# Kernel tuning notes

Measured on AMD Instinct MI355X. Metric: run time of the kernel, lower is better.

## Reference

```python
import jax, jax.numpy as jnp
import numpy as np

EPS = 1e-12
BIG_NEG = 1e10
SPARSE_RATIO = 0.5
ATTN_W = 0.8
KEEPED = 39          # int(196 * 0.4 * 0.5)
HIDDEN = 102         # int(512 * 0.2)
DIM = 512


def l2norm(x, axis=-1):
    n = jnp.sqrt(jnp.sum(x * x, axis=axis, keepdims=True))
    return x / jnp.maximum(n, EPS)


def layernorm(x, g, b):
    mu = jnp.mean(x, axis=-1, keepdims=True)
    var = jnp.mean(jnp.square(x - mu), axis=-1, keepdims=True)
    return (x - mu) / jnp.sqrt(var + 1e-5) * g + b


def token_aggregation(x, ln_g, ln_b, W1, b1, W2, b2, scale):
    # x: [B, L, C] -> [B, K, C]
    h = layernorm(x, ln_g, ln_b)
    h = jax.nn.gelu(h @ W1 + b1, approximate=False)
    w = h @ W2 + b2                       # [B, L, K]
    w = jnp.swapaxes(w, 1, 2) * scale     # [B, K, L]
    w = jax.nn.softmax(w, axis=2)
    return jnp.einsum('bkl,blc->bkc', w, x)


def setup_inputs() -> dict:
    key = jax.random.key(0)
    ks = jax.random.split(key, 8)
    B_v, L_v, B_t, L_t = 256, 197, 256, 64
    inp = {
        'img_embs': jax.random.normal(ks[0], (B_v, L_v, DIM), jnp.float32),
        'cap_embs': jax.random.normal(ks[1], (B_t, L_t, DIM), jnp.float32),
        'cap_lens': jax.random.randint(ks[2], (B_t,), 8, L_t + 1),
        'ln_g': jnp.ones((DIM,), jnp.float32),
        'ln_b': jnp.zeros((DIM,), jnp.float32),
        'W1': jax.random.normal(ks[3], (DIM, HIDDEN), jnp.float32) * 0.02,
        'b1': jnp.zeros((HIDDEN,), jnp.float32),
        'W2': jax.random.normal(ks[4], (HIDDEN, KEEPED), jnp.float32) * 0.02,
        'b2': jnp.zeros((KEEPED,), jnp.float32),
        'scale': jnp.ones((1, 1, 1), jnp.float32),
    }
    return inp


def reference(img_embs, cap_embs, cap_lens, ln_g, ln_b, W1, b1, W2, b2, scale):
    B_v = img_embs.shape[0]
    L_t = cap_embs.shape[1]
    num_keep = int(KEEPED * SPARSE_RATIO)  # 19

    # CLS split (197 is not a perfect square -> has_cls_token)
    img_cls = img_embs[:, 0:1, :]
    spatial = img_embs[:, 1:, :]

    aggr = token_aggregation(spatial, ln_g, ln_b, W1, b1, W2, b2, scale)  # [B_v, 39, C]
    aggr_norm = l2norm(aggr)
    cap_norm = l2norm(cap_embs)

    glo = jax.lax.stop_gradient(l2norm(jnp.mean(aggr, axis=1, keepdims=True)))
    att_self = jax.lax.stop_gradient(jnp.sum(glo * aggr_norm, axis=-1))  # [B_v, 39]

    word_mask = (jnp.arange(L_t)[None, :] < cap_lens[:, None]).astype(img_embs.dtype)

    def one_caption(cap_i, cap_i_norm, m):
        nw = jnp.sum(m)
        cap_glo = jax.lax.stop_gradient(
            l2norm(jnp.sum(cap_i * m[:, None], axis=0) / nw))        # [C]
        att_y = jax.lax.stop_gradient(
            jnp.sum(cap_glo * aggr_norm, axis=-1))                    # [B_v, 39]
        score = ATTN_W * att_y + (1.0 - ATTN_W) * att_self
        _, idx = jax.lax.top_k(score, num_keep)                       # [B_v, 19]
        select = jnp.take_along_axis(aggr, idx[:, :, None], axis=1)   # [B_v, 19, C]
        score_mask = jnp.zeros_like(score).at[
            jnp.arange(B_v)[:, None], idx].set(1.0)                   # [B_v, 39]
        w_drop = jax.nn.softmax(score - score_mask * BIG_NEG, axis=-1)
        extra = jnp.einsum('bl,blc->bc', w_drop, aggr)[:, None, :]    # [B_v, 1, C]
        sel = l2norm(jnp.concatenate([img_cls, select, extra], axis=1))  # [B_v, 21, C]
        sim = jnp.einsum('wc,bkc->bwk', cap_i_norm, sel)              # [B_v, L_t, 21]
        sim_max = jnp.max(sim, axis=-1)                               # [B_v, L_t]
        sim_text = jnp.sum(sim_max * m, axis=-1) / nw                 # [B_v]
        return sim_text, score_mask

    sims, score_mask_all = jax.vmap(one_caption)(cap_embs, cap_norm, word_mask)
    return sims.T  # [B_v, B_t]
```

## Files before the change

kernel.cpp:

```cpp
#include <hip/hip_runtime.h>
#include <hip/hip_bf16.h>
#include <cfloat>
#include <cmath>

typedef float f32x4 __attribute__((ext_vector_type(4)));
typedef float f32x2 __attribute__((ext_vector_type(2)));
typedef short bf16x8 __attribute__((ext_vector_type(8)));

#define HID 102
#define KEEPN 39
#define DIMD 512

static __device__ __forceinline__ unsigned int f2bf(float v) {
  unsigned int b = __float_as_uint(v);
  return (b + 0x7FFFu + ((b >> 16) & 1u)) >> 16;
}
static __device__ __forceinline__ float wsum(float v) {
#pragma unroll
  for (int m = 1; m < 64; m <<= 1) v += __shfl_xor(v, m, 64);
  return v;
}
static __device__ __forceinline__ float wmaxr(float v) {
#pragma unroll
  for (int m = 1; m < 64; m <<= 1) v = fmaxf(v, __shfl_xor(v, m, 64));
  return v;
}
static __device__ __forceinline__ float bsum(float v, float* red4, int lane, int wid) {
  v = wsum(v);
  if (lane == 0) red4[wid] = v;
  __syncthreads();
  float r = red4[0] + red4[1] + red4[2] + red4[3];
  __syncthreads();
  return r;
}

__global__ __launch_bounds__(256) void k0_prep(
    const float* __restrict__ W1, const float* __restrict__ b1,
    const float* __restrict__ W2, const float* __restrict__ lng,
    const float* __restrict__ lnb,
    float* __restrict__ w1gT, float* __restrict__ b1eff, float* __restrict__ w2T) {
  int tid = blockIdx.x * 256 + threadIdx.x;
  for (int idx = tid; idx < HID * DIMD; idx += (int)gridDim.x * 256) {
    int c = idx >> 9, k = idx & 511;
    w1gT[idx] = lng[k] * W1[k * HID + c];
  }
  for (int idx = tid; idx < KEEPN * 104; idx += (int)gridDim.x * 256) {
    int l = idx / 104, k = idx - l * 104;
    w2T[idx] = (k < HID) ? W2[k * KEEPN + l] : 0.0f;
  }
  if (blockIdx.x == 0 && threadIdx.x < 104) {
    int c = threadIdx.x;
    float s = 0.f;
    if (c < HID) {
      s = b1[c];
      for (int k = 0; k < DIMD; ++k) s += lnb[k] * W1[k * HID + c];
    }
    b1eff[c] = s;
  }
}

__global__ __launch_bounds__(256, 2) void k1a(
    const float* __restrict__ img, const float* __restrict__ w1gT,
    const float* __restrict__ b1eff, const float* __restrict__ w2T,
    const float* __restrict__ b2, const float* __restrict__ scale,
    float* __restrict__ wmat) {
  int b = blockIdx.x;
  int tid = threadIdx.x;
  int lane = tid & 63, wid = tid >> 6;
  __shared__ float mu_s[196], rs_s[196];
  __shared__ __attribute__((aligned(16))) float w2t_s[KEEPN * 104];
  __shared__ float b1e_s[104];
  __shared__ __attribute__((aligned(16))) float uni[6864];
  float* x_s = uni;
  float* w1g_s = uni + 2176;
  float* h1_s = uni;
  const float* xb = img + (size_t)b * 197 * DIMD + DIMD;
  float scv = scale[0];
  for (int u = tid; u < KEEPN * 104 / 4; u += 256)
    ((f32x4*)w2t_s)[u] = ((const f32x4*)w2T)[u];
  if (tid < 104) b1e_s[tid] = b1eff[tid];
#pragma unroll 1
  for (int it = 0; it < 49; ++it) {
    int t = it * 4 + wid;
    const float* xr = xb + (size_t)t * DIMD + lane * 8;
    f32x4 v0 = *(const f32x4*)xr;
    f32x4 v1 = *(const f32x4*)(xr + 4);
    float s = v0[0]+v0[1]+v0[2]+v0[3]+v1[0]+v1[1]+v1[2]+v1[3];
    float q = v0[0]*v0[0]+v0[1]*v0[1]+v0[2]*v0[2]+v0[3]*v0[3]
            + v1[0]*v1[0]+v1[1]*v1[1]+v1[2]*v1[2]+v1[3]*v1[3];
    s = wsum(s); q = wsum(q);
    if (lane == 0) {
      float mu = s * (1.f/512.f);
      float var = q * (1.f/512.f) - mu*mu;
      mu_s[t] = mu;
      rs_s[t] = 1.f / sqrtf(var + 1e-5f);
    }
  }
  __syncthreads();
  int kh = tid >> 7, r = tid & 127, tg = r & 15, cg = r >> 4;
#pragma unroll 1
  for (int t0 = 0; t0 < 196; t0 += 64) {
    float acc[4][13] = {};
#pragma unroll 1
    for (int kc = 0; kc < DIMD; kc += 32) {
      __syncthreads();
#pragma unroll
      for (int j = 0; j < 2; ++j) {
        int u = tid + 256 * j;
        int tt = u >> 3, f = u & 7;
        int t = t0 + tt;
        if (t < 196) {
          f32x4 v = *(const f32x4*)(xb + (size_t)t * DIMD + kc + 4*f);
          float mu = mu_s[t], rs = rs_s[t];
          x_s[(4*f+0)*68 + tt] = (v[0]-mu)*rs;
          x_s[(4*f+1)*68 + tt] = (v[1]-mu)*rs;
          x_s[(4*f+2)*68 + tt] = (v[2]-mu)*rs;
          x_s[(4*f+3)*68 + tt] = (v[3]-mu)*rs;
        }
      }
#pragma unroll
      for (int j = 0; j < 4; ++j) {
        int u = tid + 256 * j;
        if (u < 816) {
          int c = u >> 3, f = u & 7;
          *(f32x4*)&w1g_s[c*36 + 4*f] = *(const f32x4*)(w1gT + c*DIMD + kc + 4*f);
        }
      }
      __syncthreads();
#pragma unroll
      for (int k4 = 0; k4 < 4; ++k4) {
        int kk = kh*16 + k4*4;
        f32x4 a0 = *(const f32x4*)&x_s[(kk+0)*68 + 4*tg];
        f32x4 a1 = *(const f32x4*)&x_s[(kk+1)*68 + 4*tg];
        f32x4 a2 = *(const f32x4*)&x_s[(kk+2)*68 + 4*tg];
        f32x4 a3 = *(const f32x4*)&x_s[(kk+3)*68 + 4*tg];
#pragma unroll
        for (int ci = 0; ci < 13; ++ci) {
          f32x4 w = *(const f32x4*)&w1g_s[(cg*13+ci)*36 + kk];
#pragma unroll
          for (int t = 0; t < 4; ++t)
            acc[t][ci] += a0[t]*w[0] + a1[t]*w[1] + a2[t]*w[2] + a3[t]*w[3];
        }
      }
    }
    __syncthreads();
    if (kh == 1) {
#pragma unroll
      for (int ci = 0; ci < 13; ++ci) {
        int c = cg*13 + ci;
        if (c < HID)
#pragma unroll
          for (int t = 0; t < 4; ++t) h1_s[c*66 + 4*tg + t] = acc[t][ci];
      }
    }
    __syncthreads();
    if (kh == 0) {
#pragma unroll
      for (int ci = 0; ci < 13; ++ci) {
        int c = cg*13 + ci;
        if (c < HID)
#pragma unroll
          for (int t = 0; t < 4; ++t) {
            float v = h1_s[c*66 + 4*tg + t] + acc[t][ci] + b1e_s[c];
            v = 0.5f * v * (1.f + erff(v * 0.70710678118654752f));
            h1_s[c*66 + 4*tg + t] = v;
          }
      }
    }
    if (tid < 128) h1_s[(HID + (tid >> 6))*66 + (tid & 63)] = 0.f;
    __syncthreads();
    {
      int t4 = tid & 31, lg = tid >> 5;
      int nl = (lg == 7) ? 4 : 5;
      float a2c[2][5] = {};
#pragma unroll 2
      for (int k = 0; k < 104; k += 4) {
        f32x4 wvv[5];
#pragma unroll
        for (int li = 0; li < 5; ++li) {
          if (li < nl) wvv[li] = *(const f32x4*)&w2t_s[(lg*5+li)*104 + k];
          else wvv[li] = (f32x4){0.f,0.f,0.f,0.f};
        }
#pragma unroll
        for (int j = 0; j < 4; ++j) {
          f32x2 h = *(const f32x2*)&h1_s[(k+j)*66 + 2*t4];
#pragma unroll
          for (int li = 0; li < 5; ++li) {
            a2c[0][li] += h[0]*wvv[li][j];
            a2c[1][li] += h[1]*wvv[li][j];
          }
        }
      }
#pragma unroll
      for (int li = 0; li < 5; ++li) {
        if (li < nl) {
          int l = lg*5 + li;
          float bb = b2[l];
#pragma unroll
          for (int tp = 0; tp < 2; ++tp) {
            int t = t0 + 2*t4 + tp;
            if (t < 196) wmat[((size_t)b*KEEPN + l)*196 + t] = (a2c[tp][li] + bb) * scv;
          }
        }
      }
    }
  }
}

__global__ __launch_bounds__(256) void k1agg(
    const float* __restrict__ img, const float* __restrict__ wmat,
    float* __restrict__ agn, unsigned short* __restrict__ bm,
    float* __restrict__ na_g, float* __restrict__ gloraw) {
  int b = blockIdx.x, tid = threadIdx.x;
  int lane = tid & 63, wid = tid >> 6;
  __shared__ __attribute__((aligned(16))) float wm_s[KEEPN * 200];
  __shared__ float red_s[13 * 4];
  __shared__ float na_s[13];
  for (int u = tid; u < KEEPN * 49; u += 256) {
    int l = u / 49, t4 = u - l * 49;
    *(f32x4*)&wm_s[l*200 + 4*t4] = *(const f32x4*)(wmat + ((size_t)b*KEEPN + l)*196 + 4*t4);
  }
  __syncthreads();
  for (int l = wid; l < KEEPN; l += 4) {
    float v0 = wm_s[l*200 + lane];
    float v1 = wm_s[l*200 + 64 + lane];
    float v2 = wm_s[l*200 + 128 + lane];
    float v3 = (lane < 4) ? wm_s[l*200 + 192 + lane] : -FLT_MAX;
    float mx = wmaxr(fmaxf(fmaxf(v0, v1), fmaxf(v2, v3)));
    float e0 = expf(v0 - mx), e1 = expf(v1 - mx), e2 = expf(v2 - mx);
    float e3 = (lane < 4) ? expf(v3 - mx) : 0.f;
    float s = wsum(e0 + e1 + e2 + e3);
    float inv = 1.f / s;
    wm_s[l*200 + lane] = e0 * inv;
    wm_s[l*200 + 64 + lane] = e1 * inv;
    wm_s[l*200 + 128 + lane] = e2 * inv;
    if (lane < 4) wm_s[l*200 + 192 + lane] = e3 * inv;
  }
  __syncthreads();
  const float* xb = img + (size_t)b * 197 * DIMD + DIMD;
  int cc = 2 * tid;
  float ms0 = 0.f, ms1 = 0.f;
#pragma unroll 1
  for (int lp = 0; lp < 3; ++lp) {
    int l0 = lp * 13;
    float a0[13] = {}, a1[13] = {};
#pragma unroll 1
    for (int t4 = 0; t4 < 49; ++t4) {
      f32x2 xx[4];
#pragma unroll
      for (int j = 0; j < 4; ++j) {
        int t = 4*t4 + j;
        xx[j] = *(const f32x2*)(xb + (size_t)t*DIMD + cc);
      }
#pragma unroll
      for (int li = 0; li < 13; ++li) {
        f32x4 w = *(const f32x4*)&wm_s[(l0+li)*200 + 4*t4];
#pragma unroll
        for (int j = 0; j < 4; ++j) {
          a0[li] += w[j]*xx[j][0];
          a1[li] += w[j]*xx[j][1];
        }
      }
    }
#pragma unroll
    for (int li = 0; li < 13; ++li) {
      float p = wsum(a0[li]*a0[li] + a1[li]*a1[li]);
      if (lane == 0) red_s[li*4 + wid] = p;
    }
    __syncthreads();
    if (tid < 13) {
      float s = red_s[tid*4] + red_s[tid*4+1] + red_s[tid*4+2] + red_s[tid*4+3];
      float n = sqrtf(s);
      na_s[tid] = n;
      na_g[b*KEEPN + l0 + tid] = n;
    }
    __syncthreads();
#pragma unroll
    for (int li = 0; li < 13; ++li) {
      int l = l0 + li;
      float inv = 1.f / fmaxf(na_s[li], 1e-12f);
      size_t abase = ((size_t)b*KEEPN + l) * DIMD;
      size_t bbase = ((size_t)b*48 + l) * DIMD;
      float v0 = a0[li]*inv, v1 = a1[li]*inv;
      *(f32x2*)&agn[abase + cc] = (f32x2){v0, v1};
      *(unsigned int*)&bm[bbase + cc] = f2bf(v0) | (f2bf(v1) << 16);
      ms0 += a0[li]; ms1 += a1[li];
    }
    __syncthreads();
  }
  *(f32x2*)&gloraw[(size_t)b*DIMD + cc] = (f32x2){ms0, ms1};
}

__global__ __launch_bounds__(256) void k1b(
    const float* __restrict__ img, const float* __restrict__ gloraw,
    const float* __restrict__ agn, const float* __restrict__ na_g,
    unsigned short* __restrict__ bm, float* __restrict__ attSelf,
    float* __restrict__ G) {
  int b = blockIdx.x, tid = threadIdx.x;
  int lane = tid & 63, wid = tid >> 6;
  __shared__ float glo_s[DIMD];
  __shared__ float red4[4];
  int c0 = tid, c1 = tid + 256;
  float m0 = gloraw[(size_t)b*DIMD + c0] * (1.f/39.f);
  float m1 = gloraw[(size_t)b*DIMD + c1] * (1.f/39.f);
  float nt = bsum(m0*m0 + m1*m1, red4, lane, wid);
  float inv = 1.f / fmaxf(sqrtf(nt), 1e-12f);
  glo_s[c0] = m0*inv; glo_s[c1] = m1*inv;
  const float* cls = img + (size_t)b * 197 * DIMD;
  float x0 = cls[c0], x1 = cls[c1];
  float n2 = bsum(x0*x0 + x1*x1, red4, lane, wid);
  float inv2 = 1.f / fmaxf(sqrtf(n2), 1e-12f);
  bm[((size_t)b*48 + 39)*DIMD + c0] = (unsigned short)f2bf(x0*inv2);
  bm[((size_t)b*48 + 39)*DIMD + c1] = (unsigned short)f2bf(x1*inv2);
  for (int u = tid; u < 8*DIMD; u += 256) {
    int rr = u >> 9, c = u & 511;
    bm[((size_t)b*48 + 40 + rr)*DIMD + c] = 0;
  }
  __syncthreads();
#pragma unroll 1
  for (int l = 0; l < KEEPN; ++l) {
    const float* ar = agn + ((size_t)b*KEEPN + l)*DIMD;
    float p = glo_s[c0]*ar[c0] + glo_s[c1]*ar[c1];
    float s = bsum(p, red4, lane, wid);
    if (tid == 0) attSelf[b*KEEPN + l] = s;
  }
#pragma unroll 1
  for (int p = tid; p < KEEPN*KEEPN; p += 256) {
    int l = p / KEEPN, lq = p - l*KEEPN;
    const float* A = agn + ((size_t)b*KEEPN + l)*DIMD;
    const float* B = agn + ((size_t)b*KEEPN + lq)*DIMD;
    float d = 0.f;
#pragma unroll 4
    for (int c = 0; c < DIMD; c += 4) {
      f32x4 va = *(const f32x4*)(A + c);
      f32x4 vb = *(const f32x4*)(B + c);
      d += va[0]*vb[0] + va[1]*vb[1] + va[2]*vb[2] + va[3]*vb[3];
    }
    G[(size_t)b*(KEEPN*KEEPN) + p] = d * na_g[b*KEEPN + l] * na_g[b*KEEPN + lq];
  }
}

__global__ __launch_bounds__(256) void k2(
    const float* __restrict__ cap, const int* __restrict__ lens,
    unsigned short* __restrict__ capn_bf, float* __restrict__ cglo) {
  int i = blockIdx.x, tid = threadIdx.x;
  int lane = tid & 63, wid = tid >> 6;
  __shared__ float red4[4];
  int len = lens[i];
  float nwf = (float)len;
  const float* cb = cap + (size_t)i * 64 * DIMD;
  for (int w = wid; w < 64; w += 4) {
    const float* xr = cb + (size_t)w*DIMD + lane*8;
    f32x4 v0 = *(const f32x4*)xr;
    f32x4 v1 = *(const f32x4*)(xr + 4);
    float q = v0[0]*v0[0]+v0[1]*v0[1]+v0[2]*v0[2]+v0[3]*v0[3]
            + v1[0]*v1[0]+v1[1]*v1[1]+v1[2]*v1[2]+v1[3]*v1[3];
    q = wsum(q);
    float inv = 1.f / fmaxf(sqrtf(q), 1e-12f);
    uint4 o;
    o.x = f2bf(v0[0]*inv) | (f2bf(v0[1]*inv) << 16);
    o.y = f2bf(v0[2]*inv) | (f2bf(v0[3]*inv) << 16);
    o.z = f2bf(v1[0]*inv) | (f2bf(v1[1]*inv) << 16);
    o.w = f2bf(v1[2]*inv) | (f2bf(v1[3]*inv) << 16);
    *(uint4*)(capn_bf + ((size_t)i*64 + w)*DIMD + lane*8) = o;
  }
  int c0 = tid, c1 = tid + 256;
  float s0 = 0.f, s1 = 0.f;
#pragma unroll 1
  for (int w = 0; w < len; ++w) {
    s0 += cb[(size_t)w*DIMD + c0];
    s1 += cb[(size_t)w*DIMD + c1];
  }
  s0 /= nwf; s1 /= nwf;
  float nt = bsum(s0*s0 + s1*s1, red4, lane, wid);
  float inv = 1.f / fmaxf(sqrtf(nt), 1e-12f);
  cglo[(size_t)i*DIMD + c0] = s0*inv;
  cglo[(size_t)i*DIMD + c1] = s1*inv;
}

__global__ __launch_bounds__(256) void k3p(
    const float* __restrict__ agn, const float* __restrict__ cglo,
    const float* __restrict__ attSelf, const float* __restrict__ na_g,
    const float* __restrict__ G,
    float* __restrict__ wdna_g, unsigned long long* __restrict__ selmask_g,
    float* __restrict__ nexinv_g) {
  int b = blockIdx.x, igrp = blockIdx.y;
  int tid = threadIdx.x, lane = tid & 63, wv = tid >> 6;
  __shared__ __attribute__((aligned(16))) float cg_s[64*36];
  __shared__ __attribute__((aligned(16))) float ag_s[40*36];
  __shared__ float sc_s[64*40];
  __shared__ float G_s[39*33];
  __shared__ float as_s[40];
  __shared__ float na_s[40];
  int ic0 = igrp * 64;
  for (int u = tid; u < KEEPN*KEEPN; u += 256) {
    int l = u / 39, q = u - l*39;
    G_s[l*33 + q] = G[(size_t)b*(KEEPN*KEEPN) + u];
  }
  if (tid < 39) { as_s[tid] = attSelf[b*KEEPN + tid]; na_s[tid] = na_g[b*KEEPN + tid]; }
  int i2 = tid & 31, l5 = tid >> 5;
  float acc0[5] = {}, acc1[5] = {};
#pragma unroll 1
  for (int kc = 0; kc < DIMD; kc += 32) {
    __syncthreads();
#pragma unroll
    for (int j = 0; j < 2; ++j) {
      int idx = tid + 256*j;
      int r = idx >> 3, cq = idx & 7;
      *(f32x4*)&cg_s[r*36 + 4*cq] = *(const f32x4*)&cglo[(size_t)(ic0 + r)*DIMD + kc + 4*cq];
    }
    if (tid < 320) {
      int r = tid >> 3, cq = tid & 7;
      f32x4 v = {0.f,0.f,0.f,0.f};
      if (r < 39) v = *(const f32x4*)&agn[((size_t)b*KEEPN + r)*DIMD + kc + 4*cq];
      *(f32x4*)&ag_s[r*36 + 4*cq] = v;
    }
    __syncthreads();
#pragma unroll
    for (int c4 = 0; c4 < 8; ++c4) {
      f32x4 a0 = *(const f32x4*)&cg_s[i2*36 + 4*c4];
      f32x4 a1 = *(const f32x4*)&cg_s[(i2+32)*36 + 4*c4];
#pragma unroll
      for (int li = 0; li < 5; ++li) {
        f32x4 bv = *(const f32x4*)&ag_s[(l5*5+li)*36 + 4*c4];
        acc0[li] += a0[0]*bv[0]+a0[1]*bv[1]+a0[2]*bv[2]+a0[3]*bv[3];
        acc1[li] += a1[0]*bv[0]+a1[1]*bv[1]+a1[2]*bv[2]+a1[3]*bv[3];
      }
    }
  }
  __syncthreads();
#pragma unroll
  for (int li = 0; li < 5; ++li) {
    int l = l5*5 + li;
    if (l < KEEPN) {
      sc_s[i2*40 + l]      = 0.8f*acc0[li] + 0.2f*as_s[l];
      sc_s[(i2+32)*40 + l] = 0.8f*acc1[li] + 0.2f*as_s[l];
    }
  }
  __syncthreads();
#pragma unroll 1
  for (int it = 0; it < 16; ++it) {
    int ic = it*4 + wv;
    size_t pair = (size_t)b*256 + ic0 + ic;
    float sc = (lane < KEEPN) ? sc_s[ic*40 + lane] : -FLT_MAX;
    int rank = 0;
    for (int lp = 0; lp < KEEPN; ++lp) {
      float ov = __shfl(sc, lp, 64);
      if (ov > sc || (ov == sc && lp < lane)) rank++;
    }
    bool selected = (lane < KEEPN && rank < 19);
    float uv = (lane < KEEPN && !selected) ? sc : -FLT_MAX;
    float m2 = wmaxr(uv);
    float pp = (lane < KEEPN && !selected) ? expf(sc - m2) : 0.f;
    float S = wsum(pp);
    float wd = pp / S;
    float rowdot = 0.f;
    for (int lp = 0; lp < KEEPN; ++lp) {
      float wdlp = __shfl(wd, lp, 64);
      if (lane < KEEPN) rowdot += wdlp * G_s[lane*33 + lp];
    }
    float nex2 = wsum((lane < KEEPN) ? wd*rowdot : 0.f);
    unsigned long long msk = __ballot(selected) | (1ull << 39);
    if (lane < 40) wdna_g[pair*40 + lane] = (lane < KEEPN) ? wd * na_s[lane] : 0.f;
    if (lane == 0) {
      selmask_g[pair] = msk;
      nexinv_g[pair] = 1.f / fmaxf(sqrtf(fmaxf(nex2, 0.f)), 1e-12f);
    }
  }
}

__global__ __launch_bounds__(256, 2) void k3g(
    const unsigned short* __restrict__ capn_bf, const unsigned short* __restrict__ bm,
    const float* __restrict__ wdna_g, const unsigned long long* __restrict__ selmask_g,
    const float* __restrict__ nexinv_g, const int* __restrict__ lens,
    float* __restrict__ out) {
  int bid = blockIdx.x;
  int btile = bid >> 8;
  int i = bid & 255;
  int tid = threadIdx.x, lane = tid & 63, wv = tid >> 6;
  __shared__ __attribute__((aligned(16))) unsigned short A_s[64*64];
  __shared__ __attribute__((aligned(16))) unsigned short B_s[384*64];
  __shared__ float wd_s[8*48];
  __shared__ float sf_s[8*48];
  __shared__ float nx_s[8];
  int len = lens[i];
  const unsigned short* cb = capn_bf + (size_t)i * 64 * DIMD;
  const unsigned short* bb = bm + (size_t)btile * 384 * DIMD;
  for (int u = tid; u < 384; u += 256) {
    int g = u / 48, l = u - g*48;
    size_t pair = (size_t)(btile*8 + g)*256 + i;
    float wdv = 0.f, sfv = 0.f;
    if (l < 40) {
      wdv = wdna_g[pair*40 + l];
      sfv = ((selmask_g[pair] >> l) & 1ull) ? 1.f : 0.f;
    }
    wd_s[u] = wdv; sf_s[u] = sfv;
    if (l == 0) nx_s[g] = nexinv_g[pair];
  }
  f32x4 acc[4][6];
#pragma unroll
  for (int m = 0; m < 4; ++m)
#pragma unroll
    for (int n = 0; n < 6; ++n) acc[m][n] = (f32x4){0.f,0.f,0.f,0.f};
#pragma unroll 1
  for (int kc = 0; kc < 8; ++kc) {
    __syncthreads();
#pragma unroll
    for (int half = 0; half < 2; ++half) {
      uint4 vals[7];
#pragma unroll
      for (int j = 0; j < 7; ++j) {
        int u = (half*7 + j)*256 + tid;
        const unsigned short* src;
        if (u < 512) { int row = u >> 3, k8 = u & 7; src = cb + (size_t)row*DIMD + kc*64 + k8*8; }
        else { int ub = u - 512; int row = ub >> 3, k8 = ub & 7; src = bb + (size_t)row*DIMD + kc*64 + k8*8; }
        vals[j] = *(const uint4*)src;
      }
#pragma unroll
      for (int j = 0; j < 7; ++j) {
        int u = (half*7 + j)*256 + tid;
        if (u < 512) { int row = u >> 3, k8 = u & 7; *(uint4*)&A_s[row*64 + (k8 ^ (row&7))*8] = vals[j]; }
        else { int ub = u - 512; int row = ub >> 3, k8 = ub & 7; *(uint4*)&B_s[row*64 + (k8 ^ (row&7))*8] = vals[j]; }
      }
    }
    __syncthreads();
#pragma unroll
    for (int ks = 0; ks < 2; ++ks) {
      int kh = 4*ks + (lane >> 4);
      bf16x8 af[4], bfr[6];
#pragma unroll
      for (int m = 0; m < 4; ++m) {
        int row = 16*m + (lane & 15);
        af[m] = *(const bf16x8*)&A_s[row*64 + (kh ^ (row&7))*8];
      }
#pragma unroll
      for (int n = 0; n < 6; ++n) {
        int row = 16*(6*wv + n) + (lane & 15);
        bfr[n] = *(const bf16x8*)&B_s[row*64 + (kh ^ (row&7))*8];
      }
#pragma unroll
      for (int m = 0; m < 4; ++m)
#pragma unroll
        for (int n = 0; n < 6; ++n)
          acc[m][n] = __builtin_amdgcn_mfma_f32_16x16x32_bf16(af[m], bfr[n], acc[m][n], 0, 0, 0);
    }
  }
  float pv[2] = {0.f, 0.f};
#pragma unroll
  for (int jj = 0; jj < 2; ++jj) {
    int g = 2*wv + jj;
    float nxi = nx_s[g];
#pragma unroll
    for (int m = 0; m < 4; ++m) {
      f32x4 ed = {0.f,0.f,0.f,0.f};
      f32x4 ms = {-FLT_MAX,-FLT_MAX,-FLT_MAX,-FLT_MAX};
#pragma unroll
      for (int j = 0; j < 3; ++j) {
        int l = 16*j + (lane & 15);
        float wdv = wd_s[g*48 + l];
        float sfv = sf_s[g*48 + l];
        f32x4 v = acc[m][3*jj + j];
#pragma unroll
        for (int q = 0; q < 4; ++q) {
          ed[q] += wdv * v[q];
          ms[q] = fmaxf(ms[q], (sfv > 0.5f) ? v[q] : -FLT_MAX);
        }
      }
#pragma unroll
      for (int sh = 1; sh < 16; sh <<= 1) {
#pragma unroll
        for (int q = 0; q < 4; ++q) {
          ed[q] += __shfl_xor(ed[q], sh, 64);
          ms[q] = fmaxf(ms[q], __shfl_xor(ms[q], sh, 64));
        }
      }
      if ((lane & 15) == 0) {
#pragma unroll
        for (int q = 0; q < 4; ++q) {
          int r2 = 16*m + (lane >> 4)*4 + q;
          float smax = fmaxf(ms[q], ed[q]*nxi);
          pv[jj] += (r2 < len) ? smax : 0.f;
        }
      }
    }
    pv[jj] += __shfl_xor(pv[jj], 16, 64);
    pv[jj] += __shfl_xor(pv[jj], 32, 64);
  }
  if (lane == 0) {
#pragma unroll
    for (int jj = 0; jj < 2; ++jj) {
      int g = 2*wv + jj;
      out[(size_t)(btile*8 + g)*256 + i] = pv[jj] / (float)len;
    }
  }
}

extern "C" void kernel_launch(void* const* d_in, const int* in_sizes, int n_in,
                              void* d_out, int out_size, void* d_ws, size_t ws_size,
                              hipStream_t stream) {
  const float* img = (const float*)d_in[0];
  const float* cap = (const float*)d_in[1];
  const int* lens = (const int*)d_in[2];
  const float* lng = (const float*)d_in[3];
  const float* lnb = (const float*)d_in[4];
  const float* W1 = (const float*)d_in[5];
  const float* b1 = (const float*)d_in[6];
  const float* W2 = (const float*)d_in[7];
  const float* b2 = (const float*)d_in[8];
  const float* scale = (const float*)d_in[9];
  float* out = (float*)d_out;
  char* ws = (char*)d_ws;
  size_t off = 0;
  auto alloc = [&](size_t bytes) -> void* {
    void* p = ws + off;
    off += (bytes + 255) & ~(size_t)255;
    return p;
  };
  float* agn             = (float*)alloc((size_t)256*39*512*4);
  unsigned short* bm     = (unsigned short*)alloc((size_t)256*48*512*2);
  unsigned short* capn_bf = (unsigned short*)alloc((size_t)256*64*512*2);
  float* cglo    = (float*)alloc((size_t)256*512*4);
  float* gloraw  = (float*)alloc((size_t)256*512*4);
  float* na_g    = (float*)alloc((size_t)256*39*4);
  float* attSelf = (float*)alloc((size_t)256*39*4);
  float* G       = (float*)alloc((size_t)256*39*39*4);
  float* w1gT    = (float*)alloc((size_t)102*512*4);
  float* b1eff   = (float*)alloc((size_t)104*4);
  float* w2T     = (float*)alloc((size_t)39*104*4);
  float* wmat    = (float*)alloc((size_t)256*39*196*4);
  float* wdna_g  = (float*)alloc((size_t)65536*40*4);
  unsigned long long* selmask_g = (unsigned long long*)alloc((size_t)65536*8);
  float* nexinv_g = (float*)alloc((size_t)65536*4);
  (void)in_sizes; (void)n_in; (void)out_size; (void)ws_size;

  hipLaunchKernelGGL(k0_prep, dim3(64), dim3(256), 0, stream,
                     W1, b1, W2, lng, lnb, w1gT, b1eff, w2T);
  hipLaunchKernelGGL(k1a, dim3(256), dim3(256), 0, stream,
                     img, w1gT, b1eff, w2T, b2, scale, wmat);
  hipLaunchKernelGGL(k1agg, dim3(256), dim3(256), 0, stream,
                     img, wmat, agn, bm, na_g, gloraw);
  hipLaunchKernelGGL(k1b, dim3(256), dim3(256), 0, stream,
                     img, gloraw, agn, na_g, bm, attSelf, G);
  hipLaunchKernelGGL(k2, dim3(256), dim3(256), 0, stream,
                     cap, lens, capn_bf, cglo);
  hipLaunchKernelGGL(k3p, dim3(256, 4), dim3(256), 0, stream,
                     agn, cglo, attSelf, na_g, G, wdna_g, selmask_g, nexinv_g);
  hipLaunchKernelGGL(k3g, dim3(8192), dim3(256), 0, stream,
                     capn_bf, bm, wdna_g, selmask_g, nexinv_g, lens, out);
}
```

Measured before the change: 1.285 ms.

## Double-buffer caption tile in LDS and read image operand directly from global

In the main similarity GEMM kernel, the image-side B operand is no longer staged through shared memory. Each wave loads its own B fragments straight from global memory, which is possible because waves do not share B rows. The caption A tile is double-buffered in LDS with a prefetch of the next k-chunk, leaving one barrier per iteration. The shrunken LDS footprint may also raise occupancy. Separately, the attSelf dot products are now split across waves with vectorized loads and a wave reduction instead of a block reduction per row. The risk is uncoalesced or higher-latency global loads for B feeding the MFMAs directly.

```diff
diff --git a/kernel.cpp b/kernel.cpp
--- a/kernel.cpp
+++ b/kernel.cpp
@@ -318,11 +318,17 @@
   }
   __syncthreads();
 #pragma unroll 1
-  for (int l = 0; l < KEEPN; ++l) {
-    const float* ar = agn + ((size_t)b*KEEPN + l)*DIMD;
-    float p = glo_s[c0]*ar[c0] + glo_s[c1]*ar[c1];
-    float s = bsum(p, red4, lane, wid);
-    if (tid == 0) attSelf[b*KEEPN + l] = s;
+  for (int l = wid; l < KEEPN; l += 4) {
+    const float* ar = agn + ((size_t)b*KEEPN + l)*DIMD + lane*8;
+    const float* gp = glo_s + lane*8;
+    f32x4 a0 = *(const f32x4*)ar;
+    f32x4 a1 = *(const f32x4*)(ar + 4);
+    f32x4 g0 = *(const f32x4*)gp;
+    f32x4 g1 = *(const f32x4*)(gp + 4);
+    float p = a0[0]*g0[0]+a0[1]*g0[1]+a0[2]*g0[2]+a0[3]*g0[3]
+            + a1[0]*g1[0]+a1[1]*g1[1]+a1[2]*g1[2]+a1[3]*g1[3];
+    p = wsum(p);
+    if (lane == 0) attSelf[b*KEEPN + l] = p;
   }
 #pragma unroll 1
   for (int p = tid; p < KEEPN*KEEPN; p += 256) {
@@ -478,8 +484,7 @@
   int btile = bid >> 8;
   int i = bid & 255;
   int tid = threadIdx.x, lane = tid & 63, wv = tid >> 6;
-  __shared__ __attribute__((aligned(16))) unsigned short A_s[64*64];
-  __shared__ __attribute__((aligned(16))) unsigned short B_s[384*64];
+  __shared__ __attribute__((aligned(16))) unsigned short A_s[2][64*64];
   __shared__ float wd_s[8*48];
   __shared__ float sf_s[8*48];
   __shared__ float nx_s[8];
@@ -497,46 +502,42 @@
     wd_s[u] = wdv; sf_s[u] = sfv;
     if (l == 0) nx_s[g] = nexinv_g[pair];
   }
+  int srow = tid >> 3, sk8 = tid & 7;
+  int sdst0 = srow*64 + (sk8 ^ (srow & 7))*8;
+  int sdst1 = (srow+32)*64 + (sk8 ^ (srow & 7))*8;
+  {
+    uint4 v0 = *(const uint4*)(cb + (size_t)srow*DIMD + sk8*8);
+    uint4 v1 = *(const uint4*)(cb + (size_t)(srow+32)*DIMD + sk8*8);
+    *(uint4*)&A_s[0][sdst0] = v0;
+    *(uint4*)&A_s[0][sdst1] = v1;
+  }
   f32x4 acc[4][6];
 #pragma unroll
   for (int m = 0; m < 4; ++m)
 #pragma unroll
     for (int n = 0; n < 6; ++n) acc[m][n] = (f32x4){0.f,0.f,0.f,0.f};
+  __syncthreads();
+  int cur = 0;
 #pragma unroll 1
   for (int kc = 0; kc < 8; ++kc) {
-    __syncthreads();
-#pragma unroll
-    for (int half = 0; half < 2; ++half) {
-      uint4 vals[7];
-#pragma unroll
-      for (int j = 0; j < 7; ++j) {
-        int u = (half*7 + j)*256 + tid;
-        const unsigned short* src;
-        if (u < 512) { int row = u >> 3, k8 = u & 7; src = cb + (size_t)row*DIMD + kc*64 + k8*8; }
-        else { int ub = u - 512; int row = ub >> 3, k8 = ub & 7; src = bb + (size_t)row*DIMD + kc*64 + k8*8; }
-        vals[j] = *(const uint4*)src;
-      }
-#pragma unroll
-      for (int j = 0; j < 7; ++j) {
-        int u = (half*7 + j)*256 + tid;
-        if (u < 512) { int row = u >> 3, k8 = u & 7; *(uint4*)&A_s[row*64 + (k8 ^ (row&7))*8] = vals[j]; }
-        else { int ub = u - 512; int row = ub >> 3, k8 = ub & 7; *(uint4*)&B_s[row*64 + (k8 ^ (row&7))*8] = vals[j]; }
-      }
-    }
-    __syncthreads();
+    uint4 sv0, sv1;
+    if (kc < 7) {
+      sv0 = *(const uint4*)(cb + (size_t)srow*DIMD + (kc+1)*64 + sk8*8);
+      sv1 = *(const uint4*)(cb + (size_t)(srow+32)*DIMD + (kc+1)*64 + sk8*8);
+    }
 #pragma unroll
     for (int ks = 0; ks < 2; ++ks) {
       int kh = 4*ks + (lane >> 4);
       bf16x8 af[4], bfr[6];
 #pragma unroll
+      for (int n = 0; n < 6; ++n) {
+        int row = 16*(6*wv + n) + (lane & 15);
+        bfr[n] = *(const bf16x8*)(bb + (size_t)row*DIMD + kc*64 + kh*8);
+      }
+#pragma unroll
       for (int m = 0; m < 4; ++m) {
         int row = 16*m + (lane & 15);
-        af[m] = *(const bf16x8*)&A_s[row*64 + (kh ^ (row&7))*8];
-      }
-#pragma unroll
-      for (int n = 0; n < 6; ++n) {
-        int row = 16*(6*wv + n) + (lane & 15);
-        bfr[n] = *(const bf16x8*)&B_s[row*64 + (kh ^ (row&7))*8];
+        af[m] = *(const bf16x8*)&A_s[cur][row*64 + (kh ^ (row & 7))*8];
       }
 #pragma unroll
       for (int m = 0; m < 4; ++m)
@@ -544,6 +545,12 @@
         for (int n = 0; n < 6; ++n)
           acc[m][n] = __builtin_amdgcn_mfma_f32_16x16x32_bf16(af[m], bfr[n], acc[m][n], 0, 0, 0);
     }
+    if (kc < 7) {
+      *(uint4*)&A_s[cur ^ 1][sdst0] = sv0;
+      *(uint4*)&A_s[cur ^ 1][sdst1] = sv1;
+    }
+    __syncthreads();
+    cur ^= 1;
   }
   float pv[2] = {0.f, 0.f};
 #pragma unroll
```

Result: slower. 1.321 ms (+2.8%).
